# Kernel optimization log

Hardware: AMD Instinct MI355X
Metric: run time of the kernel (lower is better)

Reference implementation:

```python
import math
import jax, jax.numpy as jnp
import numpy as np

N_EMBD = 448
NUM_HEADS = 8


def setup_inputs() -> dict:
    key = jax.random.key(0)
    ks = jax.random.split(key, 6)
    B, T, C = 4, 2048, N_EMBD
    x = jax.random.normal(ks[0], (B, T, C), dtype=jnp.float32)
    # Linear weights stored as [in, out]; y = x @ W (bias-free for q/k/v).
    s = 1.0 / math.sqrt(C)
    Wq = jax.random.normal(ks[1], (C, C), dtype=jnp.float32) * s
    Wk = jax.random.normal(ks[2], (C, C), dtype=jnp.float32) * s
    Wv = jax.random.normal(ks[3], (C, C), dtype=jnp.float32) * s
    Wp = jax.random.normal(ks[4], (C, C), dtype=jnp.float32) * s
    bp = jax.random.normal(ks[5], (C,), dtype=jnp.float32) * 0.01
    return {"x": x, "Wq": Wq, "Wk": Wk, "Wv": Wv, "Wp": Wp, "bp": bp}


def reference(x, Wq, Wk, Wv, Wp, bp):
    B, T, C = x.shape
    H = NUM_HEADS
    d = C // H
    # Projections, split into heads: [B, H, T, d]
    q = (x @ Wq).reshape(B, T, H, d).transpose(0, 2, 1, 3)
    k = (x @ Wk).reshape(B, T, H, d).transpose(0, 2, 1, 3)
    v = (x @ Wv).reshape(B, T, H, d).transpose(0, 2, 1, 3)
    # NOTE: original scales by 1/sqrt(C) (full embed dim), not 1/sqrt(head_dim).
    scale = 1.0 / math.sqrt(C)
    wei = jnp.einsum("bhtd,bhsd->bhts", q, k) * scale  # [B, H, T, T]
    causal = jnp.tril(jnp.ones((T, T), dtype=bool))
    wei = jnp.where(causal, wei, -jnp.inf)
    wei = jax.nn.softmax(wei, axis=-1)
    # dropout(p=0.2) is identity in eval mode
    out = jnp.einsum("bhts,bhsd->bhtd", wei, v)  # [B, H, T, d]
    out = out.transpose(0, 2, 1, 3).reshape(B, T, C)
    return out @ Wp + bp
```

## Files before the change

### kernel.cpp

```cpp
#include <hip/hip_runtime.h>
#include <math.h>

#define NB 4
#define NT 2048
#define NC 448
#define NH 8
#define ND 56
#define NM (NB * NT)
#define SCALE 0.04724555912615705f

typedef __attribute__((ext_vector_type(8))) short bf16x8;
typedef __attribute__((ext_vector_type(4))) float f32x4;

__device__ __forceinline__ unsigned short f2bf(float f) {
    unsigned u = __float_as_uint(f);
    u += 0x7fffu + ((u >> 16) & 1u);
    return (unsigned short)(u >> 16);
}
__device__ __forceinline__ float bf2f(unsigned short h) {
    return __uint_as_float(((unsigned)h) << 16);
}

__device__ __forceinline__ void gl_lds16(const unsigned short* g, unsigned short* l) {
    __builtin_amdgcn_global_load_lds(
        (const __attribute__((address_space(1))) unsigned int*)g,
        (__attribute__((address_space(3))) unsigned int*)l,
        16, 0, 0);
}

__device__ __forceinline__ int sw_slot(int row, int u) {
    return row * 4 + (u ^ ((row >> 1) & 3));
}

__global__ __launch_bounds__(256) void conv_x_kernel(
    const float* __restrict__ x, unsigned short* __restrict__ xh,
    unsigned short* __restrict__ xl)
{
    const size_t i4 = ((size_t)blockIdx.x * 256 + threadIdx.x) * 4;
    const float4 v = *reinterpret_cast<const float4*>(x + i4);
    ushort4 h, l;
    h.x = f2bf(v.x); l.x = f2bf(v.x - bf2f(h.x));
    h.y = f2bf(v.y); l.y = f2bf(v.y - bf2f(h.y));
    h.z = f2bf(v.z); l.z = f2bf(v.z - bf2f(h.z));
    h.w = f2bf(v.w); l.w = f2bf(v.w - bf2f(h.w));
    *reinterpret_cast<ushort4*>(xh + i4) = h;
    *reinterpret_cast<ushort4*>(xl + i4) = l;
}

__global__ __launch_bounds__(256) void conv_wt_kernel(
    const float* __restrict__ Wq, const float* __restrict__ Wk,
    const float* __restrict__ Wv, const float* __restrict__ Wp,
    unsigned short* __restrict__ wth, unsigned short* __restrict__ wtl)
{
    const int z = blockIdx.z;
    const float* __restrict__ W =
        (z == 0) ? Wq : ((z == 1) ? Wk : ((z == 2) ? Wv : Wp));
    unsigned short* __restrict__ oh = wth + (size_t)z * NC * NC;
    unsigned short* __restrict__ ol = wtl + (size_t)z * NC * NC;

    __shared__ float t[32][33];
    const int tx = threadIdx.x & 31;
    const int ty = threadIdx.x >> 5;
    const int x0 = blockIdx.x * 32;
    const int y0 = blockIdx.y * 32;

    #pragma unroll
    for (int i = 0; i < 4; ++i)
        t[ty + i * 8][tx] = W[(size_t)(y0 + ty + i * 8) * NC + x0 + tx];
    __syncthreads();
    #pragma unroll
    for (int i = 0; i < 4; ++i) {
        const int n = x0 + ty + i * 8;
        const int k = y0 + tx;
        const float v = t[tx][ty + i * 8];
        const unsigned short h = f2bf(v);
        oh[(size_t)n * NC + k] = h;
        ol[(size_t)n * NC + k] = f2bf(v - bf2f(h));
    }
}

__global__ __launch_bounds__(256) void qkv_mfma_kernel(
    const unsigned short* __restrict__ xh, const unsigned short* __restrict__ xl,
    const unsigned short* __restrict__ wth, const unsigned short* __restrict__ wtl,
    unsigned short* __restrict__ qo, unsigned short* __restrict__ ko,
    unsigned short* __restrict__ vo)
{
    __shared__ unsigned short Ah[128 * 32], Al[128 * 32];
    __shared__ unsigned short Bh[3][64 * 32], Bl[3][64 * 32];
    const int tid = threadIdx.x;
    const int l  = tid & 63, w = tid >> 6;
    const int lg = l >> 4,  lr = l & 15;
    const int wr = w >> 1,  wc = w & 1;
    const int rowBase = blockIdx.y * 128;
    const int colBase = blockIdx.x * 64;

    f32x4 acc[3][4][2];
    #pragma unroll
    for (int z = 0; z < 3; ++z)
        #pragma unroll
        for (int m = 0; m < 4; ++m)
            #pragma unroll
            for (int n = 0; n < 2; ++n) acc[z][m][n] = (f32x4){0.f, 0.f, 0.f, 0.f};

    for (int k0 = 0; k0 < NC; k0 += 32) {
        __syncthreads();
        #pragma unroll
        for (int i = 0; i < 2; ++i) {
            const int p   = w * 64 + 256 * i + l;
            const int row = p >> 2, ps = p & 3;
            const int u   = ps ^ ((row >> 1) & 3);
            const size_t src = (size_t)(rowBase + row) * NC + k0 + u * 8;
            const int dst = (w * 64 + 256 * i) * 8;
            gl_lds16(xh + src, Ah + dst);
            gl_lds16(xl + src, Al + dst);
        }
        {
            const int p   = tid;
            const int row = p >> 2, ps = p & 3;
            const int u   = ps ^ ((row >> 1) & 3);
            const size_t off = (size_t)(colBase + row) * NC + k0 + u * 8;
            #pragma unroll
            for (int z = 0; z < 3; ++z) {
                const size_t src = (size_t)z * NC * NC + off;
                gl_lds16(wth + src, &Bh[z][w * 512]);
                gl_lds16(wtl + src, &Bl[z][w * 512]);
            }
        }
        __syncthreads();

        bf16x8 a_h[4], a_l[4];
        #pragma unroll
        for (int m = 0; m < 4; ++m) {
            const int row = wr * 64 + m * 16 + lr;
            const int s   = sw_slot(row, lg) * 8;
            a_h[m] = *reinterpret_cast<const bf16x8*>(Ah + s);
            a_l[m] = *reinterpret_cast<const bf16x8*>(Al + s);
        }
        #pragma unroll
        for (int z = 0; z < 3; ++z) {
            bf16x8 b_h[2], b_l[2];
            #pragma unroll
            for (int n = 0; n < 2; ++n) {
                const int row = wc * 32 + n * 16 + lr;
                const int s   = sw_slot(row, lg) * 8;
                b_h[n] = *reinterpret_cast<const bf16x8*>(&Bh[z][s]);
                b_l[n] = *reinterpret_cast<const bf16x8*>(&Bl[z][s]);
            }
            #pragma unroll
            for (int m = 0; m < 4; ++m)
                #pragma unroll
                for (int n = 0; n < 2; ++n) {
                    acc[z][m][n] = __builtin_amdgcn_mfma_f32_16x16x32_bf16(
                        a_h[m], b_h[n], acc[z][m][n], 0, 0, 0);
                    acc[z][m][n] = __builtin_amdgcn_mfma_f32_16x16x32_bf16(
                        a_h[m], b_l[n], acc[z][m][n], 0, 0, 0);
                    acc[z][m][n] = __builtin_amdgcn_mfma_f32_16x16x32_bf16(
                        a_l[m], b_h[n], acc[z][m][n], 0, 0, 0);
                }
        }
    }

    const int mW = rowBase + wr * 64;
    const int nW = colBase + wc * 32;
    #pragma unroll
    for (int z = 0; z < 3; ++z) {
        if (z < 2) {
            unsigned short* __restrict__ dst = (z == 0) ? qo : ko;
            #pragma unroll
            for (int m = 0; m < 4; ++m) {
                #pragma unroll
                for (int n = 0; n < 2; ++n) {
                    const int gcol = nW + n * 16 + lr;
                    const int h = gcol / ND, c = gcol - h * ND;
                    #pragma unroll
                    for (int r = 0; r < 4; ++r) {
                        const int grow = mW + m * 16 + lg * 4 + r;
                        const int b = grow >> 11, t = grow & (NT - 1);
                        dst[((size_t)(b * NH + h) * NT + t) * ND + c] =
                            f2bf(acc[z][m][n][r]);
                    }
                }
            }
        } else {
            #pragma unroll
            for (int m = 0; m < 4; ++m) {
                const int grow0 = mW + m * 16 + lg * 4;
                const int b = grow0 >> 11, t0 = grow0 & (NT - 1);
                #pragma unroll
                for (int n = 0; n < 2; ++n) {
                    const int gcol = nW + n * 16 + lr;
                    const int h = gcol / ND, c = gcol - h * ND;
                    ushort4 pk;
                    pk.x = f2bf(acc[z][m][n][0]); pk.y = f2bf(acc[z][m][n][1]);
                    pk.z = f2bf(acc[z][m][n][2]); pk.w = f2bf(acc[z][m][n][3]);
                    *reinterpret_cast<ushort4*>(
                        vo + ((size_t)(b * NH + h) * ND + c) * NT + t0) = pk;
                }
            }
        }
    }
}

__global__ __launch_bounds__(256) void proj_mfma_kernel(
    const unsigned short* __restrict__ ah_g, const unsigned short* __restrict__ al_g,
    const unsigned short* __restrict__ bth, const unsigned short* __restrict__ btl,
    const float* __restrict__ bias, float* __restrict__ out)
{
    __shared__ unsigned short Ah[128 * 32], Al[128 * 32];
    __shared__ unsigned short Bh[64 * 32],  Bl[64 * 32];
    const int tid = threadIdx.x;
    const int l  = tid & 63, w = tid >> 6;
    const int lg = l >> 4,  lr = l & 15;
    const int wr = w >> 1,  wc = w & 1;
    const int rowBase = blockIdx.y * 128;
    const int colBase = blockIdx.x * 64;

    f32x4 acc[4][2];
    #pragma unroll
    for (int m = 0; m < 4; ++m)
        #pragma unroll
        for (int n = 0; n < 2; ++n) acc[m][n] = (f32x4){0.f, 0.f, 0.f, 0.f};

    for (int k0 = 0; k0 < NC; k0 += 32) {
        __syncthreads();
        #pragma unroll
        for (int i = 0; i < 2; ++i) {
            const int p   = w * 64 + 256 * i + l;
            const int row = p >> 2, ps = p & 3;
            const int u   = ps ^ ((row >> 1) & 3);
            const size_t src = (size_t)(rowBase + row) * NC + k0 + u * 8;
            const int dst = (w * 64 + 256 * i) * 8;
            gl_lds16(ah_g + src, Ah + dst);
            gl_lds16(al_g + src, Al + dst);
        }
        {
            const int p   = w * 64 + l;
            const int row = p >> 2, ps = p & 3;
            const int u   = ps ^ ((row >> 1) & 3);
            const size_t src = (size_t)(colBase + row) * NC + k0 + u * 8;
            gl_lds16(bth + src, Bh + w * 512);
            gl_lds16(btl + src, Bl + w * 512);
        }
        __syncthreads();

        bf16x8 a_h[4], a_l[4], b_h[2], b_l[2];
        #pragma unroll
        for (int m = 0; m < 4; ++m) {
            const int row = wr * 64 + m * 16 + lr;
            const int s   = sw_slot(row, lg) * 8;
            a_h[m] = *reinterpret_cast<const bf16x8*>(Ah + s);
            a_l[m] = *reinterpret_cast<const bf16x8*>(Al + s);
        }
        #pragma unroll
        for (int n = 0; n < 2; ++n) {
            const int row = wc * 32 + n * 16 + lr;
            const int s   = sw_slot(row, lg) * 8;
            b_h[n] = *reinterpret_cast<const bf16x8*>(Bh + s);
            b_l[n] = *reinterpret_cast<const bf16x8*>(Bl + s);
        }
        #pragma unroll
        for (int m = 0; m < 4; ++m)
            #pragma unroll
            for (int n = 0; n < 2; ++n) {
                acc[m][n] = __builtin_amdgcn_mfma_f32_16x16x32_bf16(
                    a_h[m], b_h[n], acc[m][n], 0, 0, 0);
                acc[m][n] = __builtin_amdgcn_mfma_f32_16x16x32_bf16(
                    a_h[m], b_l[n], acc[m][n], 0, 0, 0);
                acc[m][n] = __builtin_amdgcn_mfma_f32_16x16x32_bf16(
                    a_l[m], b_h[n], acc[m][n], 0, 0, 0);
            }
    }

    const int mW = rowBase + wr * 64;
    const int nW = colBase + wc * 32;
    #pragma unroll
    for (int n = 0; n < 2; ++n) {
        const int gcol = nW + n * 16 + lr;
        const float bv = bias[gcol];
        #pragma unroll
        for (int m = 0; m < 4; ++m) {
            #pragma unroll
            for (int r = 0; r < 4; ++r) {
                const int grow = mW + m * 16 + lg * 4 + r;
                out[(size_t)grow * NC + gcol] = acc[m][n][r] + bv;
            }
        }
    }
}

__global__ __launch_bounds__(256) void attn_mfma_kernel(
    const unsigned short* __restrict__ q, const unsigned short* __restrict__ k,
    const unsigned short* __restrict__ vt,
    unsigned short* __restrict__ att_h, unsigned short* __restrict__ att_l)
{
    const int bh = blockIdx.x;
    const int qb = (gridDim.y - 1 - blockIdx.y) * 64;
    const int b  = bh >> 3;
    const int h  = bh & 7;

    const int tid = threadIdx.x;
    const int w   = tid >> 6;
    const int l   = tid & 63;
    const int lg  = l >> 4;
    const int lr  = l & 15;

    __shared__ unsigned short Ks [2][64 * 64];
    __shared__ unsigned short Vts[2][64 * 64];
    __shared__ unsigned short Pl[4][16 * 64];

    const unsigned short* __restrict__ Qg = q  + (size_t)bh * NT * ND;
    const unsigned short* __restrict__ Kg = k  + (size_t)bh * NT * ND;
    const unsigned short* __restrict__ Vg = vt + (size_t)bh * ND * NT;

    bf16x8 qf[2];
    {
        const int row = qb + w * 16 + lr;
        #pragma unroll
        for (int hh = 0; hh < 2; ++hh) {
            const int d0 = hh * 32 + lg * 8;
            bf16x8 tmp = {0, 0, 0, 0, 0, 0, 0, 0};
            if (d0 < ND)
                tmp = *reinterpret_cast<const bf16x8*>(Qg + (size_t)row * ND + d0);
            qf[hh] = tmp;
        }
    }

    const f32x4 fzero = {0.f, 0.f, 0.f, 0.f};
    f32x4 o[4];
    #pragma unroll
    for (int n = 0; n < 4; ++n) o[n] = fzero;
    float mrun[4] = {-INFINITY, -INFINITY, -INFINITY, -INFINITY};
    float lrun[4] = {0.f, 0.f, 0.f, 0.f};

    uint4 rK[2][2], rV[2][2];
    #pragma unroll
    for (int s = 0; s < 2; ++s)
        #pragma unroll
        for (int cc = 0; cc < 2; ++cc) {
            const int ch = tid + cc * 256;
            const int row = ch >> 3, u = ch & 7;
            uint4 kvv = make_uint4(0u, 0u, 0u, 0u);
            uint4 vvv = make_uint4(0u, 0u, 0u, 0u);
            if (u < 7)
                kvv = *reinterpret_cast<const uint4*>(
                    Kg + (size_t)(s * 64 + row) * ND + u * 8);
            if (row < ND)
                vvv = *reinterpret_cast<const uint4*>(
                    Vg + (size_t)row * NT + s * 64 + u * 8);
            rK[s][cc] = kvv; rV[s][cc] = vvv;
        }

    for (int kb = 0; kb <= qb; kb += 128) {
        #pragma unroll
        for (int s = 0; s < 2; ++s)
            #pragma unroll
            for (int cc = 0; cc < 2; ++cc) {
                const int ch = tid + cc * 256;
                const int row = ch >> 3, u = ch & 7;
                const int sl = (row * 8 + (u ^ (row & 7))) * 8;
                *reinterpret_cast<uint4*>(&Ks[s][sl])  = rK[s][cc];
                *reinterpret_cast<uint4*>(&Vts[s][sl]) = rV[s][cc];
            }
        __syncthreads();

        if (kb + 128 <= qb) {
            #pragma unroll
            for (int s = 0; s < 2; ++s)
                #pragma unroll
                for (int cc = 0; cc < 2; ++cc) {
                    const int ch = tid + cc * 256;
                    const int row = ch >> 3, u = ch & 7;
                    uint4 kvv = make_uint4(0u, 0u, 0u, 0u);
                    uint4 vvv = make_uint4(0u, 0u, 0u, 0u);
                    if (u < 7)
                        kvv = *reinterpret_cast<const uint4*>(
                            Kg + (size_t)(kb + 128 + s * 64 + row) * ND + u * 8);
                    if (row < ND)
                        vvv = *reinterpret_cast<const uint4*>(
                            Vg + (size_t)row * NT + kb + 128 + s * 64 + u * 8);
                    rK[s][cc] = kvv; rV[s][cc] = vvv;
                }
        }

        f32x4 sc[2][4];
        __builtin_amdgcn_s_setprio(1);
        #pragma unroll
        for (int s = 0; s < 2; ++s)
            #pragma unroll
            for (int n = 0; n < 4; ++n) {
                const int krow = n * 16 + lr;
                const bf16x8 kf0 = *reinterpret_cast<const bf16x8*>(
                    &Ks[s][(krow * 8 + ((0 + lg) ^ (krow & 7))) * 8]);
                const bf16x8 kf1 = *reinterpret_cast<const bf16x8*>(
                    &Ks[s][(krow * 8 + ((4 + lg) ^ (krow & 7))) * 8]);
                f32x4 a = fzero;
                a = __builtin_amdgcn_mfma_f32_16x16x32_bf16(qf[0], kf0, a, 0, 0, 0);
                a = __builtin_amdgcn_mfma_f32_16x16x32_bf16(qf[1], kf1, a, 0, 0, 0);
                sc[s][n] = a;
            }
        __builtin_amdgcn_s_setprio(0);

        #pragma unroll
        for (int s = 0; s < 2; ++s) {
            const int kbs = kb + s * 64;
            if (kbs + 63 > qb) {
                #pragma unroll
                for (int n = 0; n < 4; ++n) {
                    const int key = kbs + n * 16 + lr;
                    #pragma unroll
                    for (int r = 0; r < 4; ++r) {
                        const int qr = qb + w * 16 + lg * 4 + r;
                        if (key > qr) sc[s][n][r] = -1e30f;
                    }
                }
            }
        }

        float alpha[4];
        #pragma unroll
        for (int r = 0; r < 4; ++r) {
            float tmax = fmaxf(
                fmaxf(fmaxf(sc[0][0][r], sc[0][1][r]), fmaxf(sc[0][2][r], sc[0][3][r])),
                fmaxf(fmaxf(sc[1][0][r], sc[1][1][r]), fmaxf(sc[1][2][r], sc[1][3][r])));
            tmax = fmaxf(tmax, __shfl_xor(tmax, 1));
            tmax = fmaxf(tmax, __shfl_xor(tmax, 2));
            tmax = fmaxf(tmax, __shfl_xor(tmax, 4));
            tmax = fmaxf(tmax, __shfl_xor(tmax, 8));
            const float mnew = fmaxf(mrun[r], tmax);
            const float c = SCALE * mnew;
            alpha[r] = __expf(fmaf(SCALE, mrun[r], -c));
            mrun[r]  = mnew;
            float tsum = 0.f;
            #pragma unroll
            for (int s = 0; s < 2; ++s)
                #pragma unroll
                for (int n = 0; n < 4; ++n) {
                    const float p = __expf(fmaf(SCALE, sc[s][n][r], -c));
                    sc[s][n][r] = p;
                    tsum += p;
                }
            tsum += __shfl_xor(tsum, 1);
            tsum += __shfl_xor(tsum, 2);
            tsum += __shfl_xor(tsum, 4);
            tsum += __shfl_xor(tsum, 8);
            lrun[r] = lrun[r] * alpha[r] + tsum;
        }
        #pragma unroll
        for (int n = 0; n < 4; ++n)
            #pragma unroll
            for (int r = 0; r < 4; ++r) o[n][r] *= alpha[r];

        unsigned short* Pw = Pl[w];
        #pragma unroll
        for (int s = 0; s < 2; ++s) {
            #pragma unroll
            for (int n = 0; n < 4; ++n) {
                const int u = n * 2 + (lr >> 3);
                #pragma unroll
                for (int r = 0; r < 4; ++r) {
                    const int prow = lg * 4 + r;
                    Pw[(prow * 8 + (u ^ (prow & 7))) * 8 + (lr & 7)] =
                        f2bf(sc[s][n][r]);
                }
            }
            const bf16x8 pf0 = *reinterpret_cast<const bf16x8*>(
                &Pw[(lr * 8 + ((0 + lg) ^ (lr & 7))) * 8]);
            const bf16x8 pf1 = *reinterpret_cast<const bf16x8*>(
                &Pw[(lr * 8 + ((4 + lg) ^ (lr & 7))) * 8]);
            __builtin_amdgcn_s_setprio(1);
            #pragma unroll
            for (int n = 0; n < 4; ++n) {
                const int vrow = n * 16 + lr;
                const bf16x8 vf0 = *reinterpret_cast<const bf16x8*>(
                    &Vts[s][(vrow * 8 + ((0 + lg) ^ (vrow & 7))) * 8]);
                const bf16x8 vf1 = *reinterpret_cast<const bf16x8*>(
                    &Vts[s][(vrow * 8 + ((4 + lg) ^ (vrow & 7))) * 8]);
                o[n] = __builtin_amdgcn_mfma_f32_16x16x32_bf16(pf0, vf0, o[n], 0, 0, 0);
                o[n] = __builtin_amdgcn_mfma_f32_16x16x32_bf16(pf1, vf1, o[n], 0, 0, 0);
            }
            __builtin_amdgcn_s_setprio(0);
        }
        __syncthreads();
    }

    #pragma unroll
    for (int r = 0; r < 4; ++r) {
        const float inv = 1.0f / lrun[r];
        const int trow = qb + w * 16 + lg * 4 + r;
        const size_t rbase = ((size_t)b * NT + trow) * NC + h * ND;
        #pragma unroll
        for (int n = 0; n < 4; ++n) {
            const int c = n * 16 + lr;
            if (c < ND) {
                const float val = o[n][r] * inv;
                const unsigned short hh = f2bf(val);
                att_h[rbase + c] = hh;
                att_l[rbase + c] = f2bf(val - bf2f(hh));
            }
        }
    }
}

extern "C" void kernel_launch(void* const* d_in, const int* in_sizes, int n_in,
                              void* d_out, int out_size, void* d_ws, size_t ws_size,
                              hipStream_t stream)
{
    const float* x  = (const float*)d_in[0];
    const float* Wq = (const float*)d_in[1];
    const float* Wk = (const float*)d_in[2];
    const float* Wv = (const float*)d_in[3];
    const float* Wp = (const float*)d_in[4];
    const float* bp = (const float*)d_in[5];
    float* out = (float*)d_out;

    const size_t BTC = (size_t)NM * NC;
    const size_t WSZ = (size_t)NC * NC;
    unsigned short* p = (unsigned short*)d_ws;
    unsigned short* xh  = p;            p += BTC;
    unsigned short* xl  = p;            p += BTC;
    unsigned short* wth = p;            p += 4 * WSZ;
    unsigned short* wtl = p;            p += 4 * WSZ;
    unsigned short* qw  = p;            p += BTC;
    unsigned short* kw  = p;            p += BTC;
    unsigned short* vtw = p;            p += BTC;
    unsigned short* ath = p;            p += BTC;
    unsigned short* atl = p;            p += BTC;

    dim3 blk(256);
    conv_x_kernel<<<dim3((unsigned)(BTC / 1024)), blk, 0, stream>>>(x, xh, xl);
    conv_wt_kernel<<<dim3(NC / 32, NC / 32, 4), blk, 0, stream>>>(
        Wq, Wk, Wv, Wp, wth, wtl);
    qkv_mfma_kernel<<<dim3(NC / 64, NM / 128), blk, 0, stream>>>(
        xh, xl, wth, wtl, qw, kw, vtw);
    attn_mfma_kernel<<<dim3(NB * NH, NT / 64), blk, 0, stream>>>(
        qw, kw, vtw, ath, atl);
    proj_mfma_kernel<<<dim3(NC / 64, NM / 128, 1), blk, 0, stream>>>(
        ath, atl, wth + 3 * WSZ, wtl + 3 * WSZ, bp, out);
}
```

Baseline: 215.8 us.

## Transpose attention MFMA orientation so each lane owns one query row

Swaps the MFMA operand order so the score tile is S^T: each lane now holds scores for a single query row across four keys. Row max and sum then need only two cross-lane shuffles instead of four per row, and there is one scalar running max/sum per lane instead of four. P is packed with v_cvt_pk_bf16_f32 into 32-bit LDS words with a swizzled layout, and the output is written as ushort4 vector stores instead of scalar ones. The cost is a trickier LDS indexing scheme and more reliance on the exact MFMA lane layout.

Measured after the change: 202.1 us. 1.07x faster.

```diff
diff --git a/kernel.cpp b/kernel.cpp
--- a/kernel.cpp
+++ b/kernel.cpp
@@ -306,7 +306,7 @@
 
     __shared__ unsigned short Ks [2][64 * 64];
     __shared__ unsigned short Vts[2][64 * 64];
-    __shared__ unsigned short Pl[4][16 * 64];
+    __shared__ unsigned int   Pt[4][16 * 32];
 
     const unsigned short* __restrict__ Qg = q  + (size_t)bh * NT * ND;
     const unsigned short* __restrict__ Kg = k  + (size_t)bh * NT * ND;
@@ -329,8 +329,9 @@
     f32x4 o[4];
     #pragma unroll
     for (int n = 0; n < 4; ++n) o[n] = fzero;
-    float mrun[4] = {-INFINITY, -INFINITY, -INFINITY, -INFINITY};
-    float lrun[4] = {0.f, 0.f, 0.f, 0.f};
+    float mrun = -INFINITY;
+    float lrun = 0.f;
+    const int qr = qb + w * 16 + lr;
 
     uint4 rK[2][2], rV[2][2];
     #pragma unroll
@@ -394,8 +395,8 @@
                 const bf16x8 kf1 = *reinterpret_cast<const bf16x8*>(
                     &Ks[s][(krow * 8 + ((4 + lg) ^ (krow & 7))) * 8]);
                 f32x4 a = fzero;
-                a = __builtin_amdgcn_mfma_f32_16x16x32_bf16(qf[0], kf0, a, 0, 0, 0);
-                a = __builtin_amdgcn_mfma_f32_16x16x32_bf16(qf[1], kf1, a, 0, 0, 0);
+                a = __builtin_amdgcn_mfma_f32_16x16x32_bf16(kf0, qf[0], a, 0, 0, 0);
+                a = __builtin_amdgcn_mfma_f32_16x16x32_bf16(kf1, qf[1], a, 0, 0, 0);
                 sc[s][n] = a;
             }
         __builtin_amdgcn_s_setprio(0);
@@ -405,98 +406,98 @@
             const int kbs = kb + s * 64;
             if (kbs + 63 > qb) {
                 #pragma unroll
-                for (int n = 0; n < 4; ++n) {
-                    const int key = kbs + n * 16 + lr;
+                for (int n = 0; n < 4; ++n)
                     #pragma unroll
                     for (int r = 0; r < 4; ++r) {
-                        const int qr = qb + w * 16 + lg * 4 + r;
+                        const int key = kbs + n * 16 + lg * 4 + r;
                         if (key > qr) sc[s][n][r] = -1e30f;
                     }
-                }
-            }
-        }
-
-        float alpha[4];
-        #pragma unroll
-        for (int r = 0; r < 4; ++r) {
-            float tmax = fmaxf(
-                fmaxf(fmaxf(sc[0][0][r], sc[0][1][r]), fmaxf(sc[0][2][r], sc[0][3][r])),
-                fmaxf(fmaxf(sc[1][0][r], sc[1][1][r]), fmaxf(sc[1][2][r], sc[1][3][r])));
-            tmax = fmaxf(tmax, __shfl_xor(tmax, 1));
-            tmax = fmaxf(tmax, __shfl_xor(tmax, 2));
-            tmax = fmaxf(tmax, __shfl_xor(tmax, 4));
-            tmax = fmaxf(tmax, __shfl_xor(tmax, 8));
-            const float mnew = fmaxf(mrun[r], tmax);
-            const float c = SCALE * mnew;
-            alpha[r] = __expf(fmaf(SCALE, mrun[r], -c));
-            mrun[r]  = mnew;
-            float tsum = 0.f;
-            #pragma unroll
-            for (int s = 0; s < 2; ++s)
-                #pragma unroll
-                for (int n = 0; n < 4; ++n) {
+            }
+        }
+
+        float tm[8];
+        #pragma unroll
+        for (int s = 0; s < 2; ++s)
+            #pragma unroll
+            for (int n = 0; n < 4; ++n)
+                tm[s * 4 + n] = fmaxf(fmaxf(sc[s][n][0], sc[s][n][1]),
+                                      fmaxf(sc[s][n][2], sc[s][n][3]));
+        float tmax = fmaxf(fmaxf(fmaxf(tm[0], tm[1]), fmaxf(tm[2], tm[3])),
+                           fmaxf(fmaxf(tm[4], tm[5]), fmaxf(tm[6], tm[7])));
+        tmax = fmaxf(tmax, __shfl_xor(tmax, 16));
+        tmax = fmaxf(tmax, __shfl_xor(tmax, 32));
+        const float mnew = fmaxf(mrun, tmax);
+        const float c = SCALE * mnew;
+        const float alpha = __expf(fmaf(SCALE, mrun, -c));
+        mrun = mnew;
+        float tsum = 0.f;
+        #pragma unroll
+        for (int s = 0; s < 2; ++s)
+            #pragma unroll
+            for (int n = 0; n < 4; ++n)
+                #pragma unroll
+                for (int r = 0; r < 4; ++r) {
                     const float p = __expf(fmaf(SCALE, sc[s][n][r], -c));
                     sc[s][n][r] = p;
                     tsum += p;
                 }
-            tsum += __shfl_xor(tsum, 1);
-            tsum += __shfl_xor(tsum, 2);
-            tsum += __shfl_xor(tsum, 4);
-            tsum += __shfl_xor(tsum, 8);
-            lrun[r] = lrun[r] * alpha[r] + tsum;
-        }
+        tsum += __shfl_xor(tsum, 16);
+        tsum += __shfl_xor(tsum, 32);
+        lrun = lrun * alpha + tsum;
         #pragma unroll
         for (int n = 0; n < 4; ++n)
             #pragma unroll
-            for (int r = 0; r < 4; ++r) o[n][r] *= alpha[r];
-
-        unsigned short* Pw = Pl[w];
+            for (int r = 0; r < 4; ++r) o[n][r] *= alpha;
+
+        unsigned int* Pw = Pt[w];
         #pragma unroll
         for (int s = 0; s < 2; ++s) {
             #pragma unroll
-            for (int n = 0; n < 4; ++n) {
-                const int u = n * 2 + (lr >> 3);
-                #pragma unroll
-                for (int r = 0; r < 4; ++r) {
-                    const int prow = lg * 4 + r;
-                    Pw[(prow * 8 + (u ^ (prow & 7))) * 8 + (lr & 7)] =
-                        f2bf(sc[s][n][r]);
-                }
-            }
-            const bf16x8 pf0 = *reinterpret_cast<const bf16x8*>(
-                &Pw[(lr * 8 + ((0 + lg) ^ (lr & 7))) * 8]);
-            const bf16x8 pf1 = *reinterpret_cast<const bf16x8*>(
-                &Pw[(lr * 8 + ((4 + lg) ^ (lr & 7))) * 8]);
+            for (int np = 0; np < 4; ++np)
+                #pragma unroll
+                for (int hh = 0; hh < 2; ++hh) {
+                    unsigned int pk;
+                    asm("v_cvt_pk_bf16_f32 %0, %1, %2"
+                        : "=v"(pk)
+                        : "v"(sc[s][np][2 * hh]), "v"(sc[s][np][2 * hh + 1]));
+                    const int word = np * 8 + lg * 2 + hh;
+                    const int phys = ((word >> 2) ^ (lr & 7)) * 4 + (word & 3);
+                    Pw[lr * 32 + phys] = pk;
+                }
             __builtin_amdgcn_s_setprio(1);
             #pragma unroll
-            for (int n = 0; n < 4; ++n) {
-                const int vrow = n * 16 + lr;
-                const bf16x8 vf0 = *reinterpret_cast<const bf16x8*>(
-                    &Vts[s][(vrow * 8 + ((0 + lg) ^ (vrow & 7))) * 8]);
-                const bf16x8 vf1 = *reinterpret_cast<const bf16x8*>(
-                    &Vts[s][(vrow * 8 + ((4 + lg) ^ (vrow & 7))) * 8]);
-                o[n] = __builtin_amdgcn_mfma_f32_16x16x32_bf16(pf0, vf0, o[n], 0, 0, 0);
-                o[n] = __builtin_amdgcn_mfma_f32_16x16x32_bf16(pf1, vf1, o[n], 0, 0, 0);
+            for (int ks = 0; ks < 2; ++ks) {
+                const bf16x8 pb = *reinterpret_cast<const bf16x8*>(
+                    &Pw[lr * 32 + (((ks * 4 + lg) ^ (lr & 7)) * 4)]);
+                #pragma unroll
+                for (int n = 0; n < 4; ++n) {
+                    const int vrow = n * 16 + lr;
+                    const bf16x8 vf = *reinterpret_cast<const bf16x8*>(
+                        &Vts[s][(vrow * 8 + ((ks * 4 + lg) ^ (vrow & 7))) * 8]);
+                    o[n] = __builtin_amdgcn_mfma_f32_16x16x32_bf16(
+                        vf, pb, o[n], 0, 0, 0);
+                }
             }
             __builtin_amdgcn_s_setprio(0);
         }
         __syncthreads();
     }
 
-    #pragma unroll
-    for (int r = 0; r < 4; ++r) {
-        const float inv = 1.0f / lrun[r];
-        const int trow = qb + w * 16 + lg * 4 + r;
-        const size_t rbase = ((size_t)b * NT + trow) * NC + h * ND;
-        #pragma unroll
-        for (int n = 0; n < 4; ++n) {
-            const int c = n * 16 + lr;
-            if (c < ND) {
-                const float val = o[n][r] * inv;
-                const unsigned short hh = f2bf(val);
-                att_h[rbase + c] = hh;
-                att_l[rbase + c] = f2bf(val - bf2f(hh));
-            }
+    const float inv = 1.0f / lrun;
+    const size_t rbase = ((size_t)b * NT + qr) * NC + h * ND;
+    #pragma unroll
+    for (int n = 0; n < 4; ++n) {
+        const int d0 = n * 16 + lg * 4;
+        if (d0 < ND) {
+            float v0 = o[n][0] * inv, v1 = o[n][1] * inv;
+            float v2 = o[n][2] * inv, v3 = o[n][3] * inv;
+            ushort4 ph, pl;
+            ph.x = f2bf(v0); pl.x = f2bf(v0 - bf2f(ph.x));
+            ph.y = f2bf(v1); pl.y = f2bf(v1 - bf2f(ph.y));
+            ph.z = f2bf(v2); pl.z = f2bf(v2 - bf2f(ph.z));
+            ph.w = f2bf(v3); pl.w = f2bf(v3 - bf2f(ph.w));
+            *reinterpret_cast<ushort4*>(att_h + rbase + d0) = ph;
+            *reinterpret_cast<ushort4*>(att_l + rbase + d0) = pl;
         }
     }
 }
```
